# Performance work log

Hardware: AMD Instinct MI355X
Metric: run time of the kernel (lower is better)

The kernel has to match this reference:

```python
import jax, jax.numpy as jnp
import numpy as np

S = 2048      # seq_len
H = 32        # num_heads
G = 8         # num_groups (KV heads)
D = 128       # head_dim
HPG = H // G  # heads per group
MODEL = H * D


def setup_inputs() -> dict:
    rng = jax.random.key(0)
    ks = jax.random.split(rng, 6)
    return {
        "query": jax.random.normal(ks[0], (S, H, D), jnp.float32),
        "key":   jax.random.normal(ks[1], (S, G, D), jnp.float32),
        "value": jax.random.normal(ks[2], (S, G, D), jnp.float32),
        "mask":  jnp.zeros((S, S), jnp.float32),
        "w_out": jax.random.normal(ks[3], (MODEL, MODEL), jnp.float32) * (MODEL ** -0.5),
        "b_out": jnp.zeros((MODEL,), jnp.float32),
    }


def reference(query, key, value, mask, w_out, b_out):
    # NOTE: the original torch module prepares `mask` but never applies it to
    # the attention scores; we faithfully reproduce that (mask is unused).
    scale = D ** -0.5
    # [S,H,D] -> [H,S,D] -> [G,HPG,S,D]; head h = g*HPG + i (torch .view split)
    q = query.transpose(1, 0, 2).reshape(G, HPG, S, D)
    k = key.transpose(1, 0, 2)    # [G,S,D]
    v = value.transpose(1, 0, 2)  # [G,S,D]
    scores = jnp.einsum('ghqd,gkd->ghqk', q, k) * scale  # [G,HPG,S,S]
    attn = jax.nn.softmax(scores, axis=-1)
    out = jnp.einsum('ghqk,gkd->ghqd', attn, v)          # [G,HPG,S,D]
    # [G,HPG,S,D] -> [H,S,D] -> [S,H,D] -> [S, H*D]
    out = out.reshape(H, S, D).transpose(1, 0, 2).reshape(S, MODEL)
    out = out @ w_out.T + b_out                           # out_proj (Linear)
    return out.reshape(S, H, D)
```

## Files before the change

### kernel.cpp

```cpp
#include <hip/hip_runtime.h>
#include <hip/hip_bf16.h>
#include <stdint.h>

constexpr int S_ = 2048, H_ = 32, G_ = 8, HPG_ = 4, D_ = 128, MODEL_ = 4096;

typedef __attribute__((ext_vector_type(4))) float f32x4;
typedef __attribute__((ext_vector_type(16))) float f32x16;
typedef __attribute__((ext_vector_type(8))) short bf16x8;
typedef __attribute__((ext_vector_type(4))) short bf16x4;

__device__ inline unsigned short f2bf(float f) {
  unsigned u = __float_as_uint(f);
  u += 0x7FFFu + ((u >> 16) & 1u);
  return (unsigned short)(u >> 16);
}

__device__ inline unsigned cvt_pk_bf16(float lo, float hi) {
  unsigned r;
  asm("v_cvt_pk_bf16_f32 %0, %1, %2" : "=v"(r) : "v"(lo), "v"(hi));
  return r;
}

__device__ inline void gload_lds16(const void* g, void* l) {
  __builtin_amdgcn_global_load_lds(
      (const __attribute__((address_space(1))) unsigned int*)g,
      (__attribute__((address_space(3))) unsigned int*)l,
      16, 0, 0);
}

__global__ __launch_bounds__(256) void cvt_f32_to_bf16(
    const float* __restrict__ in, unsigned short* __restrict__ out, int n4) {
  int i = blockIdx.x * 256 + threadIdx.x;
  if (i < n4) {
    float4 v = reinterpret_cast<const float4*>(in)[i];
    bf16x4 o;
    o[0] = f2bf(v.x); o[1] = f2bf(v.y); o[2] = f2bf(v.z); o[3] = f2bf(v.w);
    reinterpret_cast<bf16x4*>(out)[i] = o;
  }
}

__global__ __launch_bounds__(256) void cvt_k_kernel(
    const float* __restrict__ in, unsigned short* __restrict__ out) {
  int i = blockIdx.x * 256 + threadIdx.x;
  int d4 = i & 31, g = (i >> 5) & 7, s = i >> 8;
  float4 v = reinterpret_cast<const float4*>(in)[i];
  bf16x4 o;
  o[0] = f2bf(v.x); o[1] = f2bf(v.y); o[2] = f2bf(v.z); o[3] = f2bf(v.w);
  reinterpret_cast<bf16x4*>(out)[(g * S_ + s) * 32 + d4] = o;
}

__global__ __launch_bounds__(256) void cvt_v_kernel(
    const float* __restrict__ in, unsigned short* __restrict__ out) {
  __shared__ float t[64][33];
  int s0 = blockIdx.x * 64, d0 = blockIdx.y * 32, g = blockIdx.z;
  int tid = threadIdx.x;
#pragma unroll
  for (int p = 0; p < 2; ++p) {
    int idx = p * 256 + tid;
    int s = idx >> 3, dq = (idx & 7) * 4;
    float4 v = *reinterpret_cast<const float4*>(
        in + ((size_t)(s0 + s) * G_ + g) * D_ + d0 + dq);
    t[s][dq] = v.x; t[s][dq + 1] = v.y; t[s][dq + 2] = v.z; t[s][dq + 3] = v.w;
  }
  __syncthreads();
  int d = tid >> 3, sq = (tid & 7) * 8;
  bf16x8 o;
#pragma unroll
  for (int j = 0; j < 8; ++j) o[j] = f2bf(t[sq + j][d]);
  *reinterpret_cast<bf16x8*>(out + ((size_t)g * D_ + d0 + d) * S_ + s0 + sq) = o;
}

constexpr int QB2 = 128, KVB = 32, NT = S_ / KVB;
constexpr float RTHR = 8.0f;

__global__ __launch_bounds__(256, 3) void attn32_kernel(
    const float* __restrict__ q, const unsigned short* __restrict__ kb,
    const unsigned short* __restrict__ vtb, unsigned short* __restrict__ aout) {
  __shared__ __align__(16) char smem[49152];

  const int qt = blockIdx.x, h = blockIdx.y;
  const int g = h >> 2;
  const int tid = threadIdx.x, w = tid >> 6, lane = tid & 63;
  const int l31 = lane & 31, hi = lane >> 5;

  const float scale2 = 0.12751742354783493f;
  bf16x8 qf[8];
  {
    const int qrow = qt * QB2 + w * 32 + l31;
    const float* qp = q + ((size_t)qrow * H_ + h) * D_;
#pragma unroll
    for (int c = 0; c < 8; ++c) {
      const float* p0 = qp + c * 16 + hi * 8;
      float4 a = *(const float4*)p0;
      float4 b = *(const float4*)(p0 + 4);
      bf16x8 f;
      f[0] = f2bf(a.x * scale2); f[1] = f2bf(a.y * scale2);
      f[2] = f2bf(a.z * scale2); f[3] = f2bf(a.w * scale2);
      f[4] = f2bf(b.x * scale2); f[5] = f2bf(b.y * scale2);
      f[6] = f2bf(b.z * scale2); f[7] = f2bf(b.w * scale2);
      qf[c] = f;
    }
  }

  const unsigned short* pK[2];
  const unsigned short* pV[2];
  {
    const unsigned short* kg = kb + (size_t)g * S_ * D_;
    const unsigned short* vg = vtb + (size_t)g * D_ * S_;
#pragma unroll
    for (int j = 0; j < 2; ++j) {
      int p = (w * 2 + j) * 1024 + lane * 16;
      int kvr = p >> 8;
      pK[j] = kg + (size_t)kvr * D_ + (((p & 255) ^ ((kvr & 15) << 4)) >> 1);
      int R = p >> 8;
      int il = (p & 255) ^ ((R & 7) << 4);
      pV[j] = vg + (size_t)(R * 4 + (il >> 6)) * S_ + ((il & 63) >> 1);
    }
  }

  auto stage = [&](int t) {
    int kv0 = t * KVB;
    char* base = smem + (t % 3) * 16384;
#pragma unroll
    for (int j = 0; j < 2; ++j) {
      gload_lds16(pK[j] + (size_t)kv0 * D_, base + (w * 2 + j) * 1024);
      gload_lds16(pV[j] + kv0, base + 8192 + (w * 2 + j) * 1024);
    }
  };

  f32x16 of[4];
#pragma unroll
  for (int i = 0; i < 4; ++i) of[i] = (f32x16)0.f;
  float m = -1e30f, l = 0.f;

  stage(0);
  stage(1);

  for (int t = 0; t < NT; ++t) {
    if (t + 1 < NT) asm volatile("s_waitcnt vmcnt(4)" ::: "memory");
    else            asm volatile("s_waitcnt vmcnt(0)" ::: "memory");
    __builtin_amdgcn_s_barrier();
    if (t + 2 < NT) stage(t + 2);

    const char* Kd = smem + (t % 3) * 16384;
    const char* Vd = Kd + 8192;

    f32x16 s0 = (f32x16)0.f, s1 = (f32x16)0.f;
    __builtin_amdgcn_s_setprio(1);
#pragma unroll
    for (int c = 0; c < 8; ++c) {
      unsigned off = (unsigned)(l31 * 256) +
                     (((unsigned)(c * 32 + hi * 16)) ^ ((unsigned)(l31 & 15) << 4));
      bf16x8 kf = *(const bf16x8*)(Kd + off);
      if (c & 1)
        s1 = __builtin_amdgcn_mfma_f32_32x32x16_bf16(kf, qf[c], s1, 0, 0, 0);
      else
        s0 = __builtin_amdgcn_mfma_f32_32x32x16_bf16(kf, qf[c], s0, 0, 0, 0);
    }
    __builtin_amdgcn_s_setprio(0);
    f32x16 sv = s0 + s1;

    float tmax = fmaxf(
        fmaxf(fmaxf(fmaxf(sv[0], sv[8]), fmaxf(sv[4], sv[12])),
              fmaxf(fmaxf(sv[1], sv[9]), fmaxf(sv[5], sv[13]))),
        fmaxf(fmaxf(fmaxf(sv[2], sv[10]), fmaxf(sv[6], sv[14])),
              fmaxf(fmaxf(sv[3], sv[11]), fmaxf(sv[7], sv[15]))));
    tmax = fmaxf(tmax, __shfl_xor(tmax, 32));
    if (__any(tmax > m + RTHR)) {
      float mnew = fmaxf(m, tmax);
      float alpha = __builtin_exp2f(m - mnew);
#pragma unroll
      for (int i = 0; i < 4; ++i)
#pragma unroll
        for (int r = 0; r < 16; ++r) of[i][r] *= alpha;
      l *= alpha;
      m = mnew;
    }
    unsigned pk[8];
    float sum = 0.f;
#pragma unroll
    for (int b = 0; b < 8; ++b) {
      float p0 = __builtin_exp2f(sv[2 * b] - m);
      float p1 = __builtin_exp2f(sv[2 * b + 1] - m);
      sum += p0 + p1;
      pk[b] = cvt_pk_bf16(p0, p1);
    }
    sum += __shfl_xor(sum, 32);
    l += sum;

    bf16x8 pf[2];
#pragma unroll
    for (int kc = 0; kc < 2; ++kc) {
      auto sA = __builtin_amdgcn_permlane32_swap(pk[kc * 4 + 0], pk[kc * 4 + 2],
                                                 false, false);
      auto sB = __builtin_amdgcn_permlane32_swap(pk[kc * 4 + 1], pk[kc * 4 + 3],
                                                 false, false);
      unsigned fr[4] = {(unsigned)sA[0], (unsigned)sB[0],
                        (unsigned)sA[1], (unsigned)sB[1]};
      __builtin_memcpy(&pf[kc], fr, 16);
    }

    __builtin_amdgcn_s_setprio(1);
#pragma unroll
    for (int db = 0; db < 4; ++db) {
      int R = db * 8 + (l31 >> 2);
      unsigned lg = (unsigned)((l31 & 3) * 64);
#pragma unroll
      for (int kc = 0; kc < 2; ++kc) {
        unsigned off = (unsigned)(R * 256) +
                       ((lg + (unsigned)(kc * 32 + hi * 16)) ^ ((unsigned)(R & 7) << 4));
        bf16x8 vf = *(const bf16x8*)(Vd + off);
        of[db] = __builtin_amdgcn_mfma_f32_32x32x16_bf16(vf, pf[kc], of[db], 0, 0, 0);
      }
    }
    __builtin_amdgcn_s_setprio(0);
  }

  __syncthreads();
  float inv = 1.0f / l;
  unsigned short* Ol = (unsigned short*)smem;
  const int ql = w * 32 + l31;
#pragma unroll
  for (int db = 0; db < 4; ++db) {
#pragma unroll
    for (int rp = 0; rp < 8; ++rp) {
      int r0 = rp * 2;
      int d0 = db * 32 + (r0 & 3) + 8 * (r0 >> 2) + 4 * hi;
      unsigned pkv = cvt_pk_bf16(of[db][r0] * inv, of[db][r0 + 1] * inv);
      unsigned off = ((unsigned)(ql * 256 + d0 * 2)) ^ ((unsigned)(ql & 7) << 4);
      *(unsigned*)((char*)Ol + off) = pkv;
    }
  }
  __syncthreads();
  const size_t obase = ((size_t)qt * QB2) * MODEL_ + (size_t)h * D_;
#pragma unroll
  for (int pass = 0; pass < 8; ++pass) {
    int row = pass * 16 + (tid >> 4);
    int c = tid & 15;
    unsigned off = ((unsigned)(row * 256 + c * 16)) ^ ((unsigned)(row & 7) << 4);
    bf16x8 vv = *(const bf16x8*)((char*)Ol + off);
    *(bf16x8*)(aout + obase + (size_t)row * MODEL_ + c * 8) = vv;
  }
}

constexpr int BM = 128, BN = 128, BK = 64;

__global__ __launch_bounds__(256, 2) void gemm_bt_bias(
    const unsigned short* __restrict__ A, const unsigned short* __restrict__ B,
    const float* __restrict__ bias, float* __restrict__ C) {
  __shared__ unsigned short As[BM * BK];
  __shared__ unsigned short Bs[BN * BK];

  const int tid = threadIdx.x;
  const int w = tid >> 6, lane = tid & 63;
  const int wr = w >> 1, wc = w & 1;
  const int r16 = lane & 15, g4 = lane >> 4;
  const int id = blockIdx.x;
  const int lin = (id & 7) * 64 + (id >> 3);
  const int row0 = (lin & 15) * BM, col0 = (lin >> 4) * BN;

  f32x4 acc[4][4];
#pragma unroll
  for (int m = 0; m < 4; ++m)
#pragma unroll
    for (int n = 0; n < 4; ++n) acc[m][n] = (f32x4)0.f;

  for (int kt = 0; kt < MODEL_ / BK; ++kt) {
    const int k0 = kt * BK;
    __syncthreads();
#pragma unroll
    for (int j = 0; j < 4; ++j) {
      int chunk = w * 4 + j;
      int sb = chunk * 1024 + lane * 16;
      int srow = sb >> 7;
      int lb = sb ^ ((srow & 7) << 4);
      int kk = (lb & 127) >> 1;
      gload_lds16(A + (size_t)(row0 + srow) * MODEL_ + k0 + kk,
                  (char*)As + chunk * 1024);
      gload_lds16(B + (size_t)(col0 + srow) * MODEL_ + k0 + kk,
                  (char*)Bs + chunk * 1024);
    }
    asm volatile("s_waitcnt vmcnt(0)" ::: "memory");
    __syncthreads();

#pragma unroll
    for (int kc = 0; kc < 2; ++kc) {
      bf16x8 af[4], bfr[4];
#pragma unroll
      for (int m = 0; m < 4; ++m) {
        int row = wr * 64 + m * 16 + r16;
        unsigned off = ((unsigned)(row * 128 + (kc * 32 + g4 * 8) * 2)) ^ ((row & 7) << 4);
        af[m] = *(bf16x8*)((char*)As + off);
      }
#pragma unroll
      for (int n = 0; n < 4; ++n) {
        int row = wc * 64 + n * 16 + r16;
        unsigned off = ((unsigned)(row * 128 + (kc * 32 + g4 * 8) * 2)) ^ ((row & 7) << 4);
        bfr[n] = *(bf16x8*)((char*)Bs + off);
      }
#pragma unroll
      for (int m = 0; m < 4; ++m)
#pragma unroll
        for (int n = 0; n < 4; ++n)
          acc[m][n] = __builtin_amdgcn_mfma_f32_16x16x32_bf16(af[m], bfr[n], acc[m][n], 0, 0, 0);
    }
  }

#pragma unroll
  for (int n = 0; n < 4; ++n) {
    int col = col0 + wc * 64 + n * 16 + r16;
    float bv = bias[col];
#pragma unroll
    for (int m = 0; m < 4; ++m) {
      int rbase = row0 + wr * 64 + m * 16 + g4 * 4;
#pragma unroll
      for (int j = 0; j < 4; ++j)
        C[(size_t)(rbase + j) * MODEL_ + col] = acc[m][n][j] + bv;
    }
  }
}

extern "C" void kernel_launch(void* const* d_in, const int* in_sizes, int n_in,
                              void* d_out, int out_size, void* d_ws, size_t ws_size,
                              hipStream_t stream) {
  const float* q = (const float*)d_in[0];
  const float* k = (const float*)d_in[1];
  const float* v = (const float*)d_in[2];
  const float* w_out = (const float*)d_in[4];
  const float* b_out = (const float*)d_in[5];
  float* out = (float*)d_out;

  unsigned short* attn_bf = (unsigned short*)d_ws;
  unsigned short* xreg = attn_bf + (size_t)S_ * MODEL_;
  unsigned short* k_bf = xreg;
  unsigned short* vt_bf = xreg + (size_t)G_ * S_ * D_;
  unsigned short* w_bf = xreg;
  if (ws_size < ((size_t)S_ * MODEL_ + (size_t)MODEL_ * MODEL_) * 2) return;

  cvt_k_kernel<<<S_ * G_ * D_ / 4 / 256, 256, 0, stream>>>(k, k_bf);
  dim3 vg(S_ / 64, D_ / 32, G_);
  cvt_v_kernel<<<vg, 256, 0, stream>>>(v, vt_bf);

  dim3 ag(S_ / QB2, H_);
  attn32_kernel<<<ag, 256, 0, stream>>>(q, k_bf, vt_bf, attn_bf);

  cvt_f32_to_bf16<<<(MODEL_ * MODEL_ / 4) / 256, 256, 0, stream>>>(
      w_out, w_bf, MODEL_ * MODEL_ / 4);

  gemm_bt_bias<<<512, 256, 0, stream>>>(attn_bf, w_bf, b_out, out);
}
```

Before: 192.7 us.

## Rewrite attention with 16x16x32 MFMA tiles and 8 waves per block

The flash-attention kernel switches from 32x32x16 to 16x16x32 bf16 MFMA, with each of 8 waves (512 threads) handling 16 query rows instead of 4 waves handling 32. This removes the permlane32 swap needed to build the P operand and shrinks per-thread accumulator and Q registers. Each thread now issues a single K/V async load per stage. The trade-off is more waves sharing the same KV tile, with more LDS reads per FLOP and more shuffles in the row reductions.

New measurement: 197.5 us. +2.5%, slower.

```diff
diff --git a/kernel.cpp b/kernel.cpp
--- a/kernel.cpp
+++ b/kernel.cpp
@@ -5,7 +5,6 @@
 constexpr int S_ = 2048, H_ = 32, G_ = 8, HPG_ = 4, D_ = 128, MODEL_ = 4096;
 
 typedef __attribute__((ext_vector_type(4))) float f32x4;
-typedef __attribute__((ext_vector_type(16))) float f32x16;
 typedef __attribute__((ext_vector_type(8))) short bf16x8;
 typedef __attribute__((ext_vector_type(4))) short bf16x4;
 
@@ -73,7 +72,7 @@
 constexpr int QB2 = 128, KVB = 32, NT = S_ / KVB;
 constexpr float RTHR = 8.0f;
 
-__global__ __launch_bounds__(256, 3) void attn32_kernel(
+__global__ __launch_bounds__(512, 2) void attn16_kernel(
     const float* __restrict__ q, const unsigned short* __restrict__ kb,
     const unsigned short* __restrict__ vtb, unsigned short* __restrict__ aout) {
   __shared__ __align__(16) char smem[49152];
@@ -81,63 +80,64 @@
   const int qt = blockIdx.x, h = blockIdx.y;
   const int g = h >> 2;
   const int tid = threadIdx.x, w = tid >> 6, lane = tid & 63;
-  const int l31 = lane & 31, hi = lane >> 5;
+  const int a = lane & 15, gr = lane >> 4;
+  const int kvA = 8 * (a >> 2) + (a & 3);
+  const int kvB = kvA + 4;
 
   const float scale2 = 0.12751742354783493f;
-  bf16x8 qf[8];
+  bf16x8 qf[4];
   {
-    const int qrow = qt * QB2 + w * 32 + l31;
-    const float* qp = q + ((size_t)qrow * H_ + h) * D_;
-#pragma unroll
-    for (int c = 0; c < 8; ++c) {
-      const float* p0 = qp + c * 16 + hi * 8;
-      float4 a = *(const float4*)p0;
-      float4 b = *(const float4*)(p0 + 4);
+    const int qrow = qt * QB2 + w * 16 + a;
+    const float* qp = q + ((size_t)qrow * H_ + h) * D_ + gr * 8;
+#pragma unroll
+    for (int c = 0; c < 4; ++c) {
+      float4 x = *(const float4*)(qp + c * 32);
+      float4 y = *(const float4*)(qp + c * 32 + 4);
       bf16x8 f;
-      f[0] = f2bf(a.x * scale2); f[1] = f2bf(a.y * scale2);
-      f[2] = f2bf(a.z * scale2); f[3] = f2bf(a.w * scale2);
-      f[4] = f2bf(b.x * scale2); f[5] = f2bf(b.y * scale2);
-      f[6] = f2bf(b.z * scale2); f[7] = f2bf(b.w * scale2);
+      f[0] = f2bf(x.x * scale2); f[1] = f2bf(x.y * scale2);
+      f[2] = f2bf(x.z * scale2); f[3] = f2bf(x.w * scale2);
+      f[4] = f2bf(y.x * scale2); f[5] = f2bf(y.y * scale2);
+      f[6] = f2bf(y.z * scale2); f[7] = f2bf(y.w * scale2);
       qf[c] = f;
     }
   }
 
-  const unsigned short* pK[2];
-  const unsigned short* pV[2];
+  const unsigned short* pK;
+  const unsigned short* pV;
   {
     const unsigned short* kg = kb + (size_t)g * S_ * D_;
     const unsigned short* vg = vtb + (size_t)g * D_ * S_;
-#pragma unroll
-    for (int j = 0; j < 2; ++j) {
-      int p = (w * 2 + j) * 1024 + lane * 16;
-      int kvr = p >> 8;
-      pK[j] = kg + (size_t)kvr * D_ + (((p & 255) ^ ((kvr & 15) << 4)) >> 1);
-      int R = p >> 8;
-      int il = (p & 255) ^ ((R & 7) << 4);
-      pV[j] = vg + (size_t)(R * 4 + (il >> 6)) * S_ + ((il & 63) >> 1);
-    }
+    int p = tid * 16;
+    int kvr = p >> 8;
+    pK = kg + (size_t)kvr * D_ + (((p & 255) ^ ((kvr & 15) << 4)) >> 1);
+    int R = p >> 8;
+    int il = (p & 255) ^ ((R & 7) << 4);
+    pV = vg + (size_t)(R * 4 + (il >> 6)) * S_ + ((il & 63) >> 1);
   }
 
   auto stage = [&](int t) {
-    int kv0 = t * KVB;
     char* base = smem + (t % 3) * 16384;
-#pragma unroll
-    for (int j = 0; j < 2; ++j) {
-      gload_lds16(pK[j] + (size_t)kv0 * D_, base + (w * 2 + j) * 1024);
-      gload_lds16(pV[j] + kv0, base + 8192 + (w * 2 + j) * 1024);
-    }
+    gload_lds16(pK + (size_t)(t * KVB) * D_, base + tid * 16);
+    gload_lds16(pV + t * KVB, base + 8192 + tid * 16);
   };
 
-  f32x16 of[4];
-#pragma unroll
-  for (int i = 0; i < 4; ++i) of[i] = (f32x16)0.f;
+  f32x4 of[8];
+#pragma unroll
+  for (int i = 0; i < 8; ++i) of[i] = (f32x4)0.f;
   float m = -1e30f, l = 0.f;
+
+  const unsigned swzA = (unsigned)(kvA & 15) << 4, baseA = (unsigned)kvA * 256;
+  const unsigned swzB = (unsigned)(kvB & 15) << 4, baseB = (unsigned)kvB * 256;
+  const int a2 = a >> 2, a3 = a & 3;
+  const unsigned vO = (unsigned)(a3 * 64 + 16 * gr);
+  const unsigned vSwzE = (unsigned)a2 << 4;
+  const unsigned vSwzO = (unsigned)(4 + a2) << 4;
 
   stage(0);
   stage(1);
 
   for (int t = 0; t < NT; ++t) {
-    if (t + 1 < NT) asm volatile("s_waitcnt vmcnt(4)" ::: "memory");
+    if (t + 1 < NT) asm volatile("s_waitcnt vmcnt(2)" ::: "memory");
     else            asm volatile("s_waitcnt vmcnt(0)" ::: "memory");
     __builtin_amdgcn_s_barrier();
     if (t + 2 < NT) stage(t + 2);
@@ -145,73 +145,53 @@
     const char* Kd = smem + (t % 3) * 16384;
     const char* Vd = Kd + 8192;
 
-    f32x16 s0 = (f32x16)0.f, s1 = (f32x16)0.f;
+    f32x4 sA = (f32x4)0.f, sB = (f32x4)0.f;
     __builtin_amdgcn_s_setprio(1);
 #pragma unroll
-    for (int c = 0; c < 8; ++c) {
-      unsigned off = (unsigned)(l31 * 256) +
-                     (((unsigned)(c * 32 + hi * 16)) ^ ((unsigned)(l31 & 15) << 4));
-      bf16x8 kf = *(const bf16x8*)(Kd + off);
-      if (c & 1)
-        s1 = __builtin_amdgcn_mfma_f32_32x32x16_bf16(kf, qf[c], s1, 0, 0, 0);
-      else
-        s0 = __builtin_amdgcn_mfma_f32_32x32x16_bf16(kf, qf[c], s0, 0, 0, 0);
+    for (int c = 0; c < 4; ++c) {
+      unsigned o = (unsigned)(64 * c + 16 * gr);
+      bf16x8 kfA = *(const bf16x8*)(Kd + baseA + (o ^ swzA));
+      bf16x8 kfB = *(const bf16x8*)(Kd + baseB + (o ^ swzB));
+      sA = __builtin_amdgcn_mfma_f32_16x16x32_bf16(kfA, qf[c], sA, 0, 0, 0);
+      sB = __builtin_amdgcn_mfma_f32_16x16x32_bf16(kfB, qf[c], sB, 0, 0, 0);
     }
     __builtin_amdgcn_s_setprio(0);
-    f32x16 sv = s0 + s1;
-
-    float tmax = fmaxf(
-        fmaxf(fmaxf(fmaxf(sv[0], sv[8]), fmaxf(sv[4], sv[12])),
-              fmaxf(fmaxf(sv[1], sv[9]), fmaxf(sv[5], sv[13]))),
-        fmaxf(fmaxf(fmaxf(sv[2], sv[10]), fmaxf(sv[6], sv[14])),
-              fmaxf(fmaxf(sv[3], sv[11]), fmaxf(sv[7], sv[15]))));
+
+    float tmax = fmaxf(fmaxf(fmaxf(sA[0], sA[1]), fmaxf(sA[2], sA[3])),
+                       fmaxf(fmaxf(sB[0], sB[1]), fmaxf(sB[2], sB[3])));
+    tmax = fmaxf(tmax, __shfl_xor(tmax, 16));
     tmax = fmaxf(tmax, __shfl_xor(tmax, 32));
     if (__any(tmax > m + RTHR)) {
       float mnew = fmaxf(m, tmax);
       float alpha = __builtin_exp2f(m - mnew);
 #pragma unroll
-      for (int i = 0; i < 4; ++i)
-#pragma unroll
-        for (int r = 0; r < 16; ++r) of[i][r] *= alpha;
+      for (int i = 0; i < 8; ++i)
+#pragma unroll
+        for (int r = 0; r < 4; ++r) of[i][r] *= alpha;
       l *= alpha;
       m = mnew;
     }
-    unsigned pk[8];
-    float sum = 0.f;
-#pragma unroll
-    for (int b = 0; b < 8; ++b) {
-      float p0 = __builtin_exp2f(sv[2 * b] - m);
-      float p1 = __builtin_exp2f(sv[2 * b + 1] - m);
-      sum += p0 + p1;
-      pk[b] = cvt_pk_bf16(p0, p1);
-    }
+    float pA0 = __builtin_exp2f(sA[0] - m), pA1 = __builtin_exp2f(sA[1] - m);
+    float pA2 = __builtin_exp2f(sA[2] - m), pA3 = __builtin_exp2f(sA[3] - m);
+    float pB0 = __builtin_exp2f(sB[0] - m), pB1 = __builtin_exp2f(sB[1] - m);
+    float pB2 = __builtin_exp2f(sB[2] - m), pB3 = __builtin_exp2f(sB[3] - m);
+    float sum = ((pA0 + pA1) + (pA2 + pA3)) + ((pB0 + pB1) + (pB2 + pB3));
+    sum += __shfl_xor(sum, 16);
     sum += __shfl_xor(sum, 32);
     l += sum;
 
-    bf16x8 pf[2];
-#pragma unroll
-    for (int kc = 0; kc < 2; ++kc) {
-      auto sA = __builtin_amdgcn_permlane32_swap(pk[kc * 4 + 0], pk[kc * 4 + 2],
-                                                 false, false);
-      auto sB = __builtin_amdgcn_permlane32_swap(pk[kc * 4 + 1], pk[kc * 4 + 3],
-                                                 false, false);
-      unsigned fr[4] = {(unsigned)sA[0], (unsigned)sB[0],
-                        (unsigned)sA[1], (unsigned)sB[1]};
-      __builtin_memcpy(&pf[kc], fr, 16);
-    }
+    unsigned fr[4] = {cvt_pk_bf16(pA0, pA1), cvt_pk_bf16(pA2, pA3),
+                      cvt_pk_bf16(pB0, pB1), cvt_pk_bf16(pB2, pB3)};
+    bf16x8 pf;
+    __builtin_memcpy(&pf, fr, 16);
 
     __builtin_amdgcn_s_setprio(1);
 #pragma unroll
-    for (int db = 0; db < 4; ++db) {
-      int R = db * 8 + (l31 >> 2);
-      unsigned lg = (unsigned)((l31 & 3) * 64);
-#pragma unroll
-      for (int kc = 0; kc < 2; ++kc) {
-        unsigned off = (unsigned)(R * 256) +
-                       ((lg + (unsigned)(kc * 32 + hi * 16)) ^ ((unsigned)(R & 7) << 4));
-        bf16x8 vf = *(const bf16x8*)(Vd + off);
-        of[db] = __builtin_amdgcn_mfma_f32_32x32x16_bf16(vf, pf[kc], of[db], 0, 0, 0);
-      }
+    for (int db = 0; db < 8; ++db) {
+      unsigned base = (unsigned)((db * 4 + a2) * 256);
+      unsigned o = vO ^ ((db & 1) ? vSwzO : vSwzE);
+      bf16x8 vf = *(const bf16x8*)(Vd + base + o);
+      of[db] = __builtin_amdgcn_mfma_f32_16x16x32_bf16(vf, pf, of[db], 0, 0, 0);
     }
     __builtin_amdgcn_s_setprio(0);
   }
@@ -219,23 +199,21 @@
   __syncthreads();
   float inv = 1.0f / l;
   unsigned short* Ol = (unsigned short*)smem;
-  const int ql = w * 32 + l31;
-#pragma unroll
-  for (int db = 0; db < 4; ++db) {
-#pragma unroll
-    for (int rp = 0; rp < 8; ++rp) {
-      int r0 = rp * 2;
-      int d0 = db * 32 + (r0 & 3) + 8 * (r0 >> 2) + 4 * hi;
-      unsigned pkv = cvt_pk_bf16(of[db][r0] * inv, of[db][r0 + 1] * inv);
-      unsigned off = ((unsigned)(ql * 256 + d0 * 2)) ^ ((unsigned)(ql & 7) << 4);
-      *(unsigned*)((char*)Ol + off) = pkv;
-    }
+  const int ql = w * 16 + a;
+  const unsigned swzq = (unsigned)(ql & 7) << 4;
+#pragma unroll
+  for (int db = 0; db < 8; ++db) {
+    int d0 = db * 16 + 4 * gr;
+    unsigned pk0 = cvt_pk_bf16(of[db][0] * inv, of[db][1] * inv);
+    unsigned pk1 = cvt_pk_bf16(of[db][2] * inv, of[db][3] * inv);
+    *(unsigned*)((char*)Ol + (((unsigned)(ql * 256 + d0 * 2)) ^ swzq)) = pk0;
+    *(unsigned*)((char*)Ol + (((unsigned)(ql * 256 + (d0 + 2) * 2)) ^ swzq)) = pk1;
   }
   __syncthreads();
   const size_t obase = ((size_t)qt * QB2) * MODEL_ + (size_t)h * D_;
 #pragma unroll
-  for (int pass = 0; pass < 8; ++pass) {
-    int row = pass * 16 + (tid >> 4);
+  for (int pass = 0; pass < 4; ++pass) {
+    int row = pass * 32 + (tid >> 4);
     int c = tid & 15;
     unsigned off = ((unsigned)(row * 256 + c * 16)) ^ ((unsigned)(row & 7) << 4);
     bf16x8 vv = *(const bf16x8*)((char*)Ol + off);
@@ -342,7 +320,7 @@
   cvt_v_kernel<<<vg, 256, 0, stream>>>(v, vt_bf);
 
   dim3 ag(S_ / QB2, H_);
-  attn32_kernel<<<ag, 256, 0, stream>>>(q, k_bf, vt_bf, attn_bf);
+  attn16_kernel<<<ag, 512, 0, stream>>>(q, k_bf, vt_bf, attn_bf);
 
   cvt_f32_to_bf16<<<(MODEL_ * MODEL_ / 4) / 256, 256, 0, stream>>>(
       w_out, w_bf, MODEL_ * MODEL_ / 4);
```
